# Performance work log

Hardware: AMD Instinct MI355X
Metric: run time of the kernel (lower is better)

The kernel has to match this reference:

```python
import jax, jax.numpy as jnp
from jax import lax
import numpy as np

M, CLS, K, DL, DC, DO, BD = 87, 65, 128, 128, 128, 2048, 256
B, H, W = 256, 7, 7


def _c1(x, Wt, b):
    # 1x1 Conv2d: [B,Cin,H,W] -> [B,Cout,H,W]
    return jnp.einsum('oc,bchw->bohw', Wt, x) + b[None, :, None, None]


def _pagerank(edge, v_init, p=0.85, iters=100):
    # torch: transition = adj / adj.sum(dim=1)  (broadcast divides COLUMNS by row-sums)
    n = edge.shape[0]
    Wpr = p * edge / jnp.sum(edge, axis=1)[None, :]
    s = v_init * n                                  # [B,n,1]
    coef = (1.0 - p) / n
    def body(i, xv):
        zx = coef * jnp.sum(xv, axis=1, keepdims=True)      # z_T @ x -> [B,1,1]
        return jnp.einsum('ij,bjo->bio', Wpr, xv) + s * zx
    xv = lax.fori_loop(0, iters, body, s)
    nrm = jnp.sqrt(jnp.sum(xv * xv, axis=1, keepdims=True))  # F.normalize(dim=1)
    xv = xv / jnp.maximum(nrm, 1e-12)
    return (v_init + xv).reshape(v_init.shape[0], -1)        # [B,n]


def setup_inputs() -> dict:
    key = jax.random.key(0)
    ks = jax.random.split(key, 24)
    def w(k, shape, s=0.02):
        return jax.random.normal(k, shape, jnp.float32) * s
    rng = np.random.default_rng(0)
    A = (rng.random((M, M)) < 0.08).astype(np.float32)
    A = np.maximum(A, A.T)
    np.fill_diagonal(A, 1.0)   # symmetric adjacency with self-loops (degrees > 0)
    return {
        'x': jax.random.normal(ks[0], (B, DO, H, W), jnp.float32),
        'Wb': w(ks[1], (BD, DO)), 'bb': w(ks[2], (BD,), 0.01),
        'Wfc': w(ks[3], (CLS, BD)), 'Wfc2': w(ks[4], (CLS, BD)),
        'Wo1': w(ks[5], (4 * DL, DO)), 'bo1': w(ks[6], (4 * DL,), 0.01),
        'Wo2': w(ks[7], (DL, 4 * DL)), 'bo2': w(ks[8], (DL,), 0.01),
        'Wa': w(ks[9], (M, DL)), 'ba': w(ks[10], (M,), 0.01),
        'Wps': w(ks[11], (DC, DL)), 'bps': w(ks[12], (DC,), 0.01),
        'node_p': jax.random.uniform(ks[13], (K, M), jnp.float32, -0.1, 0.1),
        'Wg': w(ks[14], (DC, DC + K)), 'bg': w(ks[15], (DC,), 0.01),
        'Wsp': w(ks[16], (DL, DC)), 'bsp': w(ks[17], (DL,), 0.01),
        'Ws': w(ks[18], (1, DC + DL)), 'bs': w(ks[19], (1,), 0.01),
        'Wox1': w(ks[20], (4 * DL, DL)), 'box1': w(ks[21], (4 * DL,), 0.01),
        'Wox2': w(ks[22], (DO, 4 * DL)), 'box2': w(ks[23], (DO,), 0.01),
        'edge': jnp.asarray(A),
    }


def reference(x, Wb, bb, Wfc, Wfc2, Wo1, bo1, Wo2, bo2, Wa, ba, Wps, bps,
              node_p, Wg, bg, Wsp, bsp, Ws, bs, Wox1, box1, Wox2, box2, edge):
    Bsz, _, hl, wl = x.shape
    HW = hl * wl

    # global pooled branch
    x_p = jnp.mean(x, axis=(2, 3))                           # [B,2048]
    features_p = x_p @ Wb.T + bb                             # [B,256]
    pre_output = features_p @ Wfc.T                          # [B,65]
    pre_score = jax.nn.softmax(lax.stop_gradient(pre_output), axis=1)

    # personalized pagerank over the semantic graph (constant wrt grads)
    v_init = jnp.concatenate(
        [jnp.zeros((Bsz, M - CLS), x.dtype), pre_score], axis=1)[:, :, None]
    v_y = lax.stop_gradient(_pagerank(edge, v_init))         # [B,87]

    # local feature reduction 2048 -> 512 -> 128
    x_l = _c1(_c1(x, Wo1, bo1), Wo2, bo2)                    # [B,128,7,7]

    a = _c1(x_l, Wa, ba).reshape(Bsz, M, HW).transpose(0, 2, 1)   # [B,HW,87]
    ps = _c1(x_l, Wps, bps).reshape(Bsz, DC, HW)                  # [B,128,HW]
    m1 = jax.nn.relu(jnp.matmul(ps, a))                           # [B,128,87]

    # replicate torch's exact (k, B*m) reshape + flat v_y broadcast
    node = jnp.broadcast_to(node_p[None], (Bsz, K, M)).reshape(K, Bsz * M)
    node = (v_y.reshape(-1) * node).reshape(Bsz, K, M)

    g = jnp.einsum('oc,bcm->bom', Wg, jnp.concatenate([node, m1], axis=1)) \
        + bg[None, :, None]                                   # [B,128,87]

    # D^-1/2 A D^-1/2 graph propagation
    Dinv = jnp.sum(edge, axis=0) ** -0.5
    edge_norm = Dinv[:, None] * edge * Dinv[None, :]
    m2 = jax.nn.relu(jnp.einsum('bcm,mn->bcn', g, edge_norm))  # [B,128,87]

    sp = jnp.einsum('oc,bcm->bom', Wsp, m2) + bsp[None, :, None]  # [B,128,87]

    # conv_s over concat(m2_expand, x_expand) is separable: avoid the
    # [B,256,HW,87] tensor entirely (1 output channel, 1x1 kernel).
    Ws1, Ws2 = Ws[0, :DC], Ws[0, DC:]
    t_node = jnp.einsum('c,bcm->bm', Ws1, m2)                  # [B,87]
    t_pix = jnp.einsum('c,bcp->bp', Ws2, x_l.reshape(Bsz, DL, HW))  # [B,HW]
    s_logits = t_node[:, :, None] + t_pix[:, None, :] + bs[0]  # [B,87,HW]
    s_att = jax.nn.softmax(s_logits, axis=1)                   # softmax over nodes

    m3 = jax.nn.relu(jnp.matmul(sp, s_att)).reshape(Bsz, DL, hl, wl)
    m3 = _c1(_c1(m3, Wox1, box1), Wox2, box2)                  # [B,2048,7,7]

    feature_aug = jnp.mean(m3, axis=(2, 3)) @ Wb.T + bb
    features = features_p + feature_aug
    outputs2 = features @ Wfc2.T
    softmax_outputs = jax.nn.softmax(outputs2, axis=1)
    return (features, outputs2, softmax_outputs, pre_output, features_p)
```

## Files before the change

### kernel.cpp

```cpp
#include <hip/hip_runtime.h>
#include <cmath>


typedef __attribute__((ext_vector_type(8))) short short8;
typedef __attribute__((ext_vector_type(4))) short s16x4;
typedef __attribute__((ext_vector_type(4))) float f32x4;

constexpr size_t OFF_W12BF = 0;
constexpr size_t OFF_T1BF  = 131072;
constexpr size_t OFF_WBBF  = 262144;
constexpr size_t OFF_XPBF  = 524288;
constexpr size_t OFF_WAPBF = 786432;
constexpr size_t OFF_WG2BF = 800768;
constexpr size_t OFF_ENPBF = 808960;
constexpr size_t OFF_B215  = 813568;
constexpr size_t OFF_B12   = 813792;
constexpr size_t OFF_WPR   = 813920;
constexpr size_t OFF_BTMP  = 821496;
constexpr size_t OFF_WC    = 823544;
constexpr size_t OFF_BC    = 856312;
constexpr size_t OFF_VY    = 856568;
constexpr size_t OFF_NT    = 878848;
constexpr size_t OFF_PART  = 901376;

__device__ __forceinline__ unsigned short f2bf(float f) {
  unsigned u = __builtin_bit_cast(unsigned, f);
  u += 0x7fffu + ((u >> 16) & 1u);
  return (unsigned short)(u >> 16);
}
__device__ __forceinline__ float bf2f(unsigned short s) {
  return __builtin_bit_cast(float, ((unsigned)s) << 16);
}

__global__ __launch_bounds__(256) void ksetup_all(
    const float* __restrict__ Wb,  const float* __restrict__ bb,
    const float* __restrict__ Wa,  const float* __restrict__ ba,
    const float* __restrict__ Wps, const float* __restrict__ bps,
    const float* __restrict__ Wg,  const float* __restrict__ edge,
    const float* __restrict__ Wo2, const float* __restrict__ Wo1,
    const float* __restrict__ Wox2,const float* __restrict__ Wox1,
    const float* __restrict__ box1,const float* __restrict__ box2,
    const float* __restrict__ bo1, const float* __restrict__ bo2,
    float* __restrict__ ws, float* __restrict__ featp)
{
  __shared__ alignas(16) short As[64*72];
  __shared__ alignas(16) short Bs[64*72];
  int blk = blockIdx.x, tid = threadIdx.x;
  if (blk < 2048) {
    int idx = blk*256 + tid;
    ((unsigned short*)(ws+OFF_WBBF))[idx] = f2bf(Wb[idx]);
  } else if (blk < 2304) {
    int idx = (blk-2048)*256 + tid;
    featp[idx] = bb[idx & 255];
  } else if (blk < 2432) {
    int idx = (blk-2304)*256 + tid;
    ws[OFF_WC + idx] = 0.f;
  } else if (blk < 2544) {
    int idx = (blk-2432)*256 + tid;
    int r = idx >> 7, c = idx & 127;
    float v;
    if (r < 128)      v = Wps[r*128 + c];
    else if (r < 215) v = Wa[(r-128)*128 + c];
    else              v = 0.f;
    ((unsigned short*)(ws+OFF_WAPBF))[idx] = f2bf(v);
  } else if (blk < 2608) {
    int idx = (blk-2544)*256 + tid;
    int o = idx >> 7, d = idx & 127;
    ((unsigned short*)(ws+OFF_WG2BF))[idx] = f2bf(Wg[o*256 + 128 + d]);
  } else if (blk < 2644) {
    int idx = (blk-2608)*256 + tid;
    int m = idx / 96, n = idx % 96;
    float v = 0.f;
    if (m < 87 && n < 87) {
      float sm = 0.f, sn = 0.f;
      for (int k = 0; k < 87; ++k) { sm += edge[k*87+m]; sn += edge[k*87+n]; }
      v = edge[m*87+n] / sqrtf(sm*sn);
    }
    ((unsigned short*)(ws+OFF_ENPBF))[idx] = f2bf(v);
  } else if (blk < 2674) {
    int idx = (blk-2644)*256 + tid;
    if (idx < 87*87) {
      int j = idx % 87;
      float rs = 0.f;
      for (int k = 0; k < 87; ++k) rs += edge[j*87+k];
      ws[OFF_WPR + idx] = 0.85f * edge[idx] / rs;
    }
  } else if (blk == 2674) {
    if (tid < 224) {
      float v = (tid < 128) ? bps[tid] : (tid < 215 ? ba[tid-128] : 0.f);
      ws[OFF_B215 + tid] = v;
    }
  } else if (blk < 2803) {
    int gb = blk - 2675;
    const float *A, *B; unsigned short* C; int lda, ldb, ldc, i0, j0;
    if (gb < 64) {
      A = Wo2; B = Wo1; C = (unsigned short*)(ws+OFF_W12BF);
      lda = 512; ldb = 2048; ldc = 2048;
      i0 = (gb & 1)*64; j0 = (gb >> 1)*64;
    } else {
      int b2 = gb - 64;
      A = Wox2; B = Wox1; C = (unsigned short*)(ws+OFF_T1BF);
      lda = 512; ldb = 128; ldc = 128;
      i0 = (b2 >> 1)*64; j0 = (b2 & 1)*64;
    }
    int w = tid >> 6, l = tid & 63, quad = l >> 4, lane16 = l & 15;
    f32x4 acc[4];
    #pragma unroll
    for (int i = 0; i < 4; ++i) acc[i] = (f32x4)(0.f);
    for (int kc = 0; kc < 512; kc += 64) {
      for (int t = tid; t < 1024; t += 256) {
        int r = t >> 4, k4 = t & 15;
        float4 v = *(const float4*)&A[(size_t)(i0+r)*lda + kc + k4*4];
        s16x4 sv; sv[0]=(short)f2bf(v.x); sv[1]=(short)f2bf(v.y); sv[2]=(short)f2bf(v.z); sv[3]=(short)f2bf(v.w);
        *(s16x4*)&As[r*72 + k4*4] = sv;
      }
      for (int t = tid; t < 1024; t += 256) {
        int kr = t >> 4, n4 = t & 15;
        float4 v = *(const float4*)&B[(size_t)(kc+kr)*ldb + j0 + n4*4];
        Bs[(n4*4+0)*72 + kr] = (short)f2bf(v.x);
        Bs[(n4*4+1)*72 + kr] = (short)f2bf(v.y);
        Bs[(n4*4+2)*72 + kr] = (short)f2bf(v.z);
        Bs[(n4*4+3)*72 + kr] = (short)f2bf(v.w);
      }
      __syncthreads();
      #pragma unroll
      for (int ks = 0; ks < 2; ++ks) {
        short8 a = *(const short8*)&As[(w*16+lane16)*72 + ks*32 + quad*8];
        #pragma unroll
        for (int nt = 0; nt < 4; ++nt) {
          short8 b8 = *(const short8*)&Bs[(nt*16+lane16)*72 + ks*32 + quad*8];
          acc[nt] = __builtin_amdgcn_mfma_f32_16x16x32_bf16(a, b8, acc[nt], 0, 0, 0);
        }
      }
      __syncthreads();
    }
    #pragma unroll
    for (int nt = 0; nt < 4; ++nt)
      #pragma unroll
      for (int r = 0; r < 4; ++r)
        C[(size_t)(i0 + w*16 + quad*4 + r)*ldc + j0 + nt*16 + lane16] = f2bf(acc[nt][r]);
  } else {
    int vb = blk - 2803;
    int w = tid >> 6, l = tid & 63;
    if (vb < 512) {
      int o = vb*4 + w;
      float s = 0.f;
      for (int h = l; h < 512; h += 64) s += Wox2[(size_t)o*512 + h] * box1[h];
      for (int off = 32; off; off >>= 1) s += __shfl_down(s, off, 64);
      if (l == 0) ws[OFF_BTMP + o] = s + box2[o];
    } else {
      int o = (vb - 512)*4 + w;
      float s = 0.f;
      for (int h = l; h < 512; h += 64) s += Wo2[(size_t)o*512 + h] * bo1[h];
      for (int off = 32; off; off >>= 1) s += __shfl_down(s, off, 64);
      if (l == 0) ws[OFF_B12 + o] = s + bo2[o];
    }
  }
}

__global__ __launch_bounds__(512, 6) void kmain5(const float* __restrict__ x,
                                                 const short* __restrict__ w12bf,
                                                 short* __restrict__ xpbf,
                                                 float* __restrict__ part)
{
  __shared__ alignas(16) short Bt[2][64*72];
  int b = blockIdx.x, q = blockIdx.y, tid = threadIdx.x;
  int w = tid >> 6, l = tid & 63;
  int quad = l >> 4, lane16 = l & 15;
  const float* xb = x + ((size_t)b*2048 + q*512)*49;

  int p4A = tid % 13, cA = tid / 13;
  int tB = tid + 512;
  int p4B = tB % 13, cB = tB / 13;
  bool hasB = (tid < 320);

  float fA[4], fB[4];
  {
    if (p4A < 12) {
      float4 v = *(const float4*)(xb + cA*49 + p4A*4);
      fA[0]=v.x; fA[1]=v.y; fA[2]=v.z; fA[3]=v.w;
    } else fA[0] = xb[cA*49 + 48];
    if (hasB) {
      if (p4B < 12) {
        float4 v = *(const float4*)(xb + cB*49 + p4B*4);
        fB[0]=v.x; fB[1]=v.y; fB[2]=v.z; fB[3]=v.w;
      } else fB[0] = xb[cB*49 + 48];
    }
  }

  f32x4 acc[4];
  #pragma unroll
  for (int i = 0; i < 4; ++i) acc[i] = (f32x4)(0.f);

  for (int kci = 0; kci < 8; ++kci) {
    short* bt = Bt[kci & 1];
    if (p4A < 12) {
      #pragma unroll
      for (int i = 0; i < 4; ++i) bt[(p4A*4+i)*72 + cA] = (short)f2bf(fA[i]);
    } else bt[48*72 + cA] = (short)f2bf(fA[0]);
    if (hasB) {
      if (p4B < 12) {
        #pragma unroll
        for (int i = 0; i < 4; ++i) bt[(p4B*4+i)*72 + cB] = (short)f2bf(fB[i]);
      } else bt[48*72 + cB] = (short)f2bf(fB[0]);
    }
    __syncthreads();
    if (kci < 7) {
      const float* xc = xb + (size_t)(kci+1)*64*49;
      if (p4A < 12) {
        float4 v = *(const float4*)(xc + cA*49 + p4A*4);
        fA[0]=v.x; fA[1]=v.y; fA[2]=v.z; fA[3]=v.w;
      } else fA[0] = xc[cA*49 + 48];
      if (hasB) {
        if (p4B < 12) {
          float4 v = *(const float4*)(xc + cB*49 + p4B*4);
          fB[0]=v.x; fB[1]=v.y; fB[2]=v.z; fB[3]=v.w;
        } else fB[0] = xc[cB*49 + 48];
      }
    }
    const short* wr = w12bf + (size_t)(w*16 + lane16)*2048 + q*512 + kci*64 + quad*8;
    short8 a0 = *(const short8*)(wr);
    short8 a1 = *(const short8*)(wr + 32);
    #pragma unroll
    for (int ni = 0; ni < 4; ++ni) {
      const short* br = bt + (ni*16 + lane16)*72 + quad*8;
      short8 b0 = *(const short8*)(br);
      short8 b1 = *(const short8*)(br + 32);
      acc[ni] = __builtin_amdgcn_mfma_f32_16x16x32_bf16(a0, b0, acc[ni], 0, 0, 0);
      acc[ni] = __builtin_amdgcn_mfma_f32_16x16x32_bf16(a1, b1, acc[ni], 0, 0, 0);
    }
    if (tid < 64) {
      float s = 0.f;
      for (int p = 0; p < 49; ++p)
        s += bf2f((unsigned short)bt[p*72 + tid]);
      xpbf[(size_t)b*2048 + q*512 + kci*64 + tid] = (short)f2bf(s * (1.f/49.f));
    }
  }
  float* po = part + ((size_t)q*256 + b)*6656;
  #pragma unroll
  for (int ni = 0; ni < 4; ++ni) {
    int p = ni*16 + lane16;
    if (p < 49) {
      #pragma unroll
      for (int r = 0; r < 4; ++r) {
        int o = w*16 + quad*4 + r;
        po[o*52 + p] = acc[ni][r];
      }
    }
  }
}

__global__ __launch_bounds__(256) void kwcf(const float* __restrict__ Wb,
                                            const float* __restrict__ bb,
                                            const short* __restrict__ xpbf,
                                            float* __restrict__ featp,
                                            float* __restrict__ ws)
{
  __shared__ alignas(16) short As[64*72];
  __shared__ alignas(16) short Bs[64*72];
  int blk = blockIdx.x, tid = threadIdx.x;
  if (blk < 64) {
    const short* wbbf = (const short*)(ws+OFF_WBBF);
    const short* t1s  = (const short*)(ws+OFF_T1BF);
    int i0 = (blk & 3)*64, j0 = ((blk >> 2) & 1)*64, kc0 = (blk >> 3)*256;
    int w = tid >> 6, l = tid & 63, quad = l >> 4, lane16 = l & 15;
    f32x4 acc[4];
    #pragma unroll
    for (int i = 0; i < 4; ++i) acc[i] = (f32x4)(0.f);
    for (int kc = kc0; kc < kc0+256; kc += 64) {
      for (int t = tid; t < 512; t += 256) {
        int r = t >> 3, c8 = t & 7;
        *(short8*)&As[r*72 + c8*8] = *(const short8*)&wbbf[(size_t)(i0+r)*2048 + kc + c8*8];
      }
      for (int t = tid; t < 1024; t += 256) {
        int kr = t >> 4, n4 = t & 15;
        s16x4 v = *(const s16x4*)&t1s[(size_t)(kc+kr)*128 + j0 + n4*4];
        Bs[(n4*4+0)*72 + kr] = v[0];
        Bs[(n4*4+1)*72 + kr] = v[1];
        Bs[(n4*4+2)*72 + kr] = v[2];
        Bs[(n4*4+3)*72 + kr] = v[3];
      }
      __syncthreads();
      #pragma unroll
      for (int ks = 0; ks < 2; ++ks) {
        short8 a = *(const short8*)&As[(w*16+lane16)*72 + ks*32 + quad*8];
        #pragma unroll
        for (int nt = 0; nt < 4; ++nt) {
          short8 b8 = *(const short8*)&Bs[(nt*16+lane16)*72 + ks*32 + quad*8];
          acc[nt] = __builtin_amdgcn_mfma_f32_16x16x32_bf16(a, b8, acc[nt], 0, 0, 0);
        }
      }
      __syncthreads();
    }
    #pragma unroll
    for (int nt = 0; nt < 4; ++nt)
      #pragma unroll
      for (int r = 0; r < 4; ++r)
        atomicAdd(&ws[OFF_WC + (size_t)(i0 + w*16 + quad*4 + r)*128 + j0 + nt*16 + lane16], acc[nt][r]);
  } else if (blk < 128) {
    int j = (blk-64)*4 + (tid >> 6), l = tid & 63;
    float s = 0.f;
    for (int c = l; c < 2048; c += 64) s += Wb[(size_t)j*2048 + c] * ws[OFF_BTMP + c];
    for (int off = 32; off; off >>= 1) s += __shfl_down(s, off, 64);
    if (l == 0) ws[OFF_BC + j] = s + bb[j];
  } else {
    const short* wbbf = (const short*)(ws+OFF_WBBF);
    int idx = blk - 128;
    int i0 = (idx & 3)*64, j0 = ((idx >> 2) & 3)*64, kc0 = (idx >> 4)*256;
    int w = tid >> 6, l = tid & 63, quad = l >> 4, lane16 = l & 15;
    f32x4 acc[4];
    #pragma unroll
    for (int i = 0; i < 4; ++i) acc[i] = (f32x4)(0.f);
    for (int kc = kc0; kc < kc0+256; kc += 32) {
      short8 a = *(const short8*)&xpbf[(size_t)(i0 + w*16 + lane16)*2048 + kc + quad*8];
      #pragma unroll
      for (int nt = 0; nt < 4; ++nt) {
        short8 b8 = *(const short8*)&wbbf[(size_t)(j0 + nt*16 + lane16)*2048 + kc + quad*8];
        acc[nt] = __builtin_amdgcn_mfma_f32_16x16x32_bf16(a, b8, acc[nt], 0, 0, 0);
      }
    }
    #pragma unroll
    for (int nt = 0; nt < 4; ++nt)
      #pragma unroll
      for (int r = 0; r < 4; ++r)
        atomicAdd(&featp[(size_t)(i0 + w*16 + quad*4 + r)*256 + j0 + nt*16 + lane16], acc[nt][r]);
  }
}

__global__ __launch_bounds__(384) void kpr(const float* __restrict__ featp,
                                           const float* __restrict__ Wfc,
                                           const float* __restrict__ wpr,
                                           float* __restrict__ preo,
                                           float* __restrict__ vy)
{
  __shared__ alignas(16) float fpr[256];
  __shared__ alignas(16) float po[68];
  __shared__ alignas(16) float vsA[88];
  __shared__ alignas(16) float vsB[88];
  __shared__ alignas(16) float vis[88];
  __shared__ float rd[4];
  int b = blockIdx.x, tid = threadIdx.x;
  if (tid < 256) fpr[tid] = featp[b*256 + tid];
  __syncthreads();
  if (tid < 260) {
    int row = tid >> 2, p = tid & 3;
    float s = 0.f;
    const float* wr = Wfc + row*256 + p*64;
    #pragma unroll
    for (int c = 0; c < 64; c += 4) {
      float4 w4 = *(const float4*)&wr[c];
      s += w4.x*fpr[p*64+c] + w4.y*fpr[p*64+c+1] + w4.z*fpr[p*64+c+2] + w4.w*fpr[p*64+c+3];
    }
    s += __shfl_xor(s, 1, 64);
    s += __shfl_xor(s, 2, 64);
    if (p == 0) { po[row] = s; preo[b*65 + row] = s; }
  }
  __syncthreads();
  if (tid < 64) {
    float v = po[tid];
    if (tid == 0) v = fmaxf(v, po[64]);
    float mx = v;
    #pragma unroll
    for (int off = 32; off; off >>= 1) mx = fmaxf(mx, __shfl_down(mx, off, 64));
    mx = __shfl(mx, 0, 64);
    float e = expf(po[tid]-mx) + ((tid == 0) ? expf(po[64]-mx) : 0.f);
    float sm = e;
    #pragma unroll
    for (int off = 32; off; off >>= 1) sm += __shfl_down(sm, off, 64);
    if (tid == 0) { rd[0] = mx; rd[1] = 1.f/sm; }
  }
  __syncthreads();
  if (tid < 88) {
    float vin = (tid >= 22 && tid < 87) ? expf(po[tid-22]-rd[0])*rd[1] : 0.f;
    vis[tid] = vin;
    vsA[tid] = vin * 87.f;
    vsB[tid] = 0.f;
  }
  __syncthreads();
  float wrow[22];
  const int m4 = tid >> 2, pp = tid & 3;
  if (tid < 348) {
    float add = vis[m4] * 0.15f;
    #pragma unroll
    for (int jj = 0; jj < 22; ++jj) {
      int j = pp*22 + jj;
      wrow[jj] = (j < 87) ? (wpr[m4*87 + j] + add) : 0.f;
    }
  }
  for (int it = 0; it < 64; ++it) {
    const float* vc = (it & 1) ? vsB : vsA;
    float* vn = (it & 1) ? vsA : vsB;
    if (tid < 348) {
      float nv = 0.f;
      #pragma unroll
      for (int jj = 0; jj < 22; ++jj) nv += wrow[jj] * vc[pp*22 + jj];
      nv += __shfl_xor(nv, 1, 64);
      nv += __shfl_xor(nv, 2, 64);
      if (pp == 0) vn[m4] = nv;
    }
    __syncthreads();
  }
  if (tid < 64) {
    float v = vsA[tid]*vsA[tid];
    if (tid < 23) v += vsA[64+tid]*vsA[64+tid];
    #pragma unroll
    for (int off = 32; off; off >>= 1) v += __shfl_down(v, off, 64);
    if (tid == 0) rd[2] = 1.f / fmaxf(sqrtf(v), 1e-12f);
  }
  __syncthreads();
  if (tid < 87) vy[b*87 + tid] = vis[tid] + vsA[tid]*rd[2];
}

__global__ __launch_bounds__(384) void knode(const float* __restrict__ Wg,
                                             const float* __restrict__ node_p,
                                             const float* __restrict__ vy,
                                             float* __restrict__ nt)
{
  int tid = threadIdx.x;
  if (tid >= 352) return;
  int out = blockIdx.x*88 + (tid >> 2);
  int par = out / 11264;
  int r = out % 11264;
  int o = r / 88, m = r % 88;
  int p = tid & 3;
  float s = 0.f;
  if (m < 87) {
    const float* vrow = vy + (size_t)(par*128)*87 + m;
    for (int k = p*32; k < p*32+32; ++k)
      s += Wg[o*256 + k] * node_p[k*87 + m] * vrow[k*87];
  }
  s += __shfl_xor(s, 1, 64);
  s += __shfl_xor(s, 2, 64);
  if (p == 0) nt[out] = s;
}

__global__ __launch_bounds__(512) void kgraph_all(
    const float* __restrict__ part,  const float* __restrict__ b12,
    const short* __restrict__ wapbf, const float* __restrict__ b215,
    const short* __restrict__ wg2bf, const float* __restrict__ nt,
    const float* __restrict__ bg,    const short* __restrict__ enpbf,
    const float* __restrict__ Wsp,   const float* __restrict__ bsp,
    const float* __restrict__ Ws,    const float* __restrict__ wc,
    const float* __restrict__ bc,    const float* __restrict__ featp,
    const float* __restrict__ Wfc2,
    float* __restrict__ feat, float* __restrict__ out2, float* __restrict__ soft)
{
  extern __shared__ char smraw[];
  short* XT = (short*)smraw;
  short* At = XT + 8704;
  short* M1 = At + 16128;
  short* G  = M1 + 13056;
  short* M2 = G  + 13312;
  float* fb  = (float*)(M2 + 13312);
  float* wsm = fb;
  float* tnb = fb + 96;
  float* zs  = fb + 192;
  float* m3s = fb + 320;
  float* fs  = fb + 448;
  float* o2s = fb + 704;
  float* red = fb + 776;

  int b = blockIdx.x, tid = threadIdx.x;
  int w = tid >> 6, l = tid & 63, quad = l >> 4, lane16 = l & 15;

  const float* p0 = part + (size_t)b*6656;
  const float* p1 = p0 + (size_t)256*6656;
  const float* p2 = p1 + (size_t)256*6656;
  const float* p3 = p2 + (size_t)256*6656;
  for (int t = tid; t < 6656; t += 512) {
    int o = t / 52, p = t % 52;
    XT[p*136 + o] = (short)f2bf(p0[t] + p1[t] + p2[t] + p3[t] + b12[o]);
  }
  for (int t = tid; t < 1536; t += 512) {
    int p = 52 + t/128, o = t % 128;
    XT[p*136 + o] = 0;
  }
  __syncthreads();

  for (int t = w; t < 56; t += 8) {
    int mt = t >> 2, n4 = t & 3;
    f32x4 acc = (f32x4)(0.f);
    #pragma unroll
    for (int ks = 0; ks < 4; ++ks) {
      short8 a  = *(const short8*)&wapbf[(size_t)(mt*16+lane16)*128 + ks*32 + quad*8];
      short8 b8 = *(const short8*)&XT[(n4*16+lane16)*136 + ks*32 + quad*8];
      acc = __builtin_amdgcn_mfma_f32_16x16x32_bf16(a, b8, acc, 0, 0, 0);
    }
    int p = n4*16 + lane16;
    #pragma unroll
    for (int r = 0; r < 4; ++r) {
      int rr = mt*16 + quad*4 + r;
      At[rr*72 + p] = (p < 49) ? (short)f2bf(acc[r] + b215[rr]) : (short)0;
    }
  }
  __syncthreads();

  for (int t = w; t < 48; t += 8) {
    int mt = t / 8, n4 = t % 8;
    f32x4 acc = (f32x4)(0.f);
    #pragma unroll
    for (int ks = 0; ks < 2; ++ks) {
      short8 a  = *(const short8*)&At[(128 + mt*16 + lane16)*72 + ks*32 + quad*8];
      short8 b8 = *(const short8*)&At[(n4*16+lane16)*72 + ks*32 + quad*8];
      acc = __builtin_amdgcn_mfma_f32_16x16x32_bf16(a, b8, acc, 0, 0, 0);
    }
    int d = n4*16 + lane16;
    #pragma unroll
    for (int r = 0; r < 4; ++r) {
      int m = mt*16 + quad*4 + r;
      M1[m*136 + d] = (short)f2bf(fmaxf(acc[r], 0.f));
    }
  }
  __syncthreads();

  const float* ntb = nt + (size_t)(b & 1)*11264;
  for (int t = w; t < 48; t += 8) {
    int mt = t / 6, n4 = t % 6;
    f32x4 acc = (f32x4)(0.f);
    #pragma unroll
    for (int ks = 0; ks < 4; ++ks) {
      short8 a  = *(const short8*)&wg2bf[(size_t)(mt*16+lane16)*128 + ks*32 + quad*8];
      short8 b8 = *(const short8*)&M1[(n4*16+lane16)*136 + ks*32 + quad*8];
      acc = __builtin_amdgcn_mfma_f32_16x16x32_bf16(a, b8, acc, 0, 0, 0);
    }
    int m = n4*16 + lane16;
    #pragma unroll
    for (int r = 0; r < 4; ++r) {
      int o = mt*16 + quad*4 + r;
      float v = acc[r] + bg[o] + ((m < 88) ? ntb[o*88 + m] : 0.f);
      G[o*104 + m] = (short)f2bf(v);
    }
  }
  __syncthreads();

  for (int t = w; t < 48; t += 8) {
    int mt = t / 6, n4 = t % 6;
    f32x4 acc = (f32x4)(0.f);
    #pragma unroll
    for (int ks = 0; ks < 3; ++ks) {
      short8 a  = *(const short8*)&G[(mt*16+lane16)*104 + ks*32 + quad*8];
      short8 b8 = *(const short8*)&enpbf[(size_t)(n4*16+lane16)*96 + ks*32 + quad*8];
      acc = __builtin_amdgcn_mfma_f32_16x16x32_bf16(a, b8, acc, 0, 0, 0);
    }
    int n = n4*16 + lane16;
    #pragma unroll
    for (int r = 0; r < 4; ++r) {
      int c = mt*16 + quad*4 + r;
      M2[c*104 + n] = (short)f2bf(fmaxf(acc[r], 0.f));
    }
  }
  __syncthreads();

  if (tid < 348) {
    int m = tid >> 2, p = tid & 3;
    float s = 0.f;
    for (int c = p*32; c < p*32+32; ++c)
      s += Ws[c] * bf2f((unsigned short)M2[c*104 + m]);
    s += __shfl_xor(s, 1, 64);
    s += __shfl_xor(s, 2, 64);
    if (p == 0) tnb[m] = s;
  }
  __syncthreads();
  if (tid < 64) {
    float v = tnb[tid];
    if (tid < 23) v = fmaxf(v, tnb[64+tid]);
    float mx = v;
    #pragma unroll
    for (int off = 32; off; off >>= 1) mx = fmaxf(mx, __shfl_down(mx, off, 64));
    mx = __shfl(mx, 0, 64);
    float e0 = expf(tnb[tid]-mx);
    float e1 = (tid < 23) ? expf(tnb[64+tid]-mx) : 0.f;
    float sm = e0 + e1;
    #pragma unroll
    for (int off = 32; off; off >>= 1) sm += __shfl_down(sm, off, 64);
    sm = __shfl(sm, 0, 64);
    float inv = 1.f/sm;
    wsm[tid] = e0*inv;
    if (tid < 23) wsm[64+tid] = e1*inv;
  }
  __syncthreads();
  {
    int c = tid >> 2, p = tid & 3;
    float s = 0.f;
    for (int mm = p*22; mm < p*22+22 && mm < 87; ++mm)
      s += bf2f((unsigned short)M2[c*104 + mm]) * wsm[mm];
    s += __shfl_xor(s, 1, 64);
    s += __shfl_xor(s, 2, 64);
    if (p == 0) zs[c] = s;
  }
  __syncthreads();
  {
    int d = tid >> 2, p = tid & 3;
    float s = 0.f;
    for (int c = p*32; c < p*32+32; ++c) s += Wsp[d*128 + c] * zs[c];
    s += __shfl_xor(s, 1, 64);
    s += __shfl_xor(s, 2, 64);
    if (p == 0) m3s[d] = fmaxf(s + bsp[d], 0.f);
  }
  __syncthreads();

  if (tid < 256) {
    float s = 0.f;
    #pragma unroll 4
    for (int d4 = 0; d4 < 32; ++d4) {
      float4 w4 = *(const float4*)&wc[tid*128 + d4*4];
      s += w4.x*m3s[d4*4] + w4.y*m3s[d4*4+1] + w4.z*m3s[d4*4+2] + w4.w*m3s[d4*4+3];
    }
    float f = featp[b*256 + tid] + bc[tid] + s;
    fs[tid] = f;
    feat[b*256 + tid] = f;
  }
  __syncthreads();
  if (tid < 260) {
    int row = tid >> 2, p = tid & 3;
    float s = 0.f;
    for (int c = p*64; c < p*64+64; c += 4) {
      float4 w4 = *(const float4*)&Wfc2[row*256 + c];
      s += w4.x*fs[c] + w4.y*fs[c+1] + w4.z*fs[c+2] + w4.w*fs[c+3];
    }
    s += __shfl_xor(s, 1, 64);
    s += __shfl_xor(s, 2, 64);
    if (p == 0) { out2[b*65 + row] = s; o2s[row] = s; }
  }
  __syncthreads();
  if (tid < 64) {
    float v = o2s[tid];
    if (tid == 0) v = fmaxf(v, o2s[64]);
    float mx = v;
    #pragma unroll
    for (int off = 32; off; off >>= 1) mx = fmaxf(mx, __shfl_down(mx, off, 64));
    mx = __shfl(mx, 0, 64);
    float e = expf(o2s[tid]-mx) + ((tid == 0) ? expf(o2s[64]-mx) : 0.f);
    float sm = e;
    #pragma unroll
    for (int off = 32; off; off >>= 1) sm += __shfl_down(sm, off, 64);
    if (tid == 0) { red[0] = mx; red[1] = 1.f/sm; }
  }
  __syncthreads();
  if (tid < 65) soft[b*65 + tid] = expf(o2s[tid]-red[0]) * red[1];
}

extern "C" void kernel_launch(void* const* d_in, const int* in_sizes, int n_in,
                              void* d_out, int out_size, void* d_ws, size_t ws_size,
                              hipStream_t stream)
{
  (void)in_sizes; (void)n_in; (void)out_size; (void)ws_size;
  const float* x      = (const float*)d_in[0];
  const float* Wb     = (const float*)d_in[1];
  const float* bb     = (const float*)d_in[2];
  const float* Wfc    = (const float*)d_in[3];
  const float* Wfc2   = (const float*)d_in[4];
  const float* Wo1    = (const float*)d_in[5];
  const float* bo1    = (const float*)d_in[6];
  const float* Wo2    = (const float*)d_in[7];
  const float* bo2    = (const float*)d_in[8];
  const float* Wa     = (const float*)d_in[9];
  const float* ba     = (const float*)d_in[10];
  const float* Wps    = (const float*)d_in[11];
  const float* bps    = (const float*)d_in[12];
  const float* node_p = (const float*)d_in[13];
  const float* Wg     = (const float*)d_in[14];
  const float* bg     = (const float*)d_in[15];
  const float* Wsp    = (const float*)d_in[16];
  const float* bsp    = (const float*)d_in[17];
  const float* Ws     = (const float*)d_in[18];
  const float* Wox1   = (const float*)d_in[20];
  const float* box1   = (const float*)d_in[21];
  const float* Wox2   = (const float*)d_in[22];
  const float* box2   = (const float*)d_in[23];
  const float* edge   = (const float*)d_in[24];

  float* ws   = (float*)d_ws;
  float* out  = (float*)d_out;
  float* feat  = out;
  float* out2  = out + 65536;
  float* soft  = out + 82176;
  float* preo  = out + 98816;
  float* featp = out + 115456;

  ksetup_all<<<3347, 256, 0, stream>>>(Wb, bb, Wa, ba, Wps, bps, Wg, edge,
                                       Wo2, Wo1, Wox2, Wox1, box1, box2, bo1, bo2,
                                       ws, featp);
  kmain5<<<dim3(256,4), 512, 0, stream>>>(x, (const short*)(ws + OFF_W12BF),
                                          (short*)(ws + OFF_XPBF), ws + OFF_PART);
  kwcf<<<256, 256, 0, stream>>>(Wb, bb, (const short*)(ws + OFF_XPBF), featp, ws);
  kpr<<<256, 384, 0, stream>>>(featp, Wfc, ws + OFF_WPR, preo, ws + OFF_VY);
  knode<<<256, 384, 0, stream>>>(Wg, node_p, ws + OFF_VY, ws + OFF_NT);
  kgraph_all<<<256, 512, 132144, stream>>>(ws + OFF_PART, ws + OFF_B12,
                                           (const short*)(ws + OFF_WAPBF),
                                           ws + OFF_B215,
                                           (const short*)(ws + OFF_WG2BF),
                                           ws + OFF_NT, bg,
                                           (const short*)(ws + OFF_ENPBF),
                                           Wsp, bsp, Ws,
                                           ws + OFF_WC, ws + OFF_BC, featp, Wfc2,
                                           feat, out2, soft);
}
```

Baseline: 331.1 us.

## Halve kmain5 K-split, precompute pooled partial sums, vectorize setup copies

The main GEMM kernel now splits the 2048-channel reduction into 2 chunks instead of 4, so each block loops over 16 K-tiles and the downstream graph kernel sums only two partial buffers. The per-channel spatial mean is computed from per-thread partial sums stored in a small shared buffer rather than by one thread serially reading 49 bf16 values, which also avoids bf16 rounding in the pool. The setup kernel's weight conversion, bias broadcast and zeroing paths use float4/short8 vector accesses with fewer blocks. The trade-off is fewer kmain5 blocks (512 vs 1024) with a lower occupancy hint and extra shared memory, against less partial-sum traffic.

```diff
diff --git a/kernel.cpp b/kernel.cpp
--- a/kernel.cpp
+++ b/kernel.cpp
@@ -46,29 +46,39 @@
   __shared__ alignas(16) short As[64*72];
   __shared__ alignas(16) short Bs[64*72];
   int blk = blockIdx.x, tid = threadIdx.x;
-  if (blk < 2048) {
-    int idx = blk*256 + tid;
-    ((unsigned short*)(ws+OFF_WBBF))[idx] = f2bf(Wb[idx]);
-  } else if (blk < 2304) {
-    int idx = (blk-2048)*256 + tid;
-    featp[idx] = bb[idx & 255];
-  } else if (blk < 2432) {
-    int idx = (blk-2304)*256 + tid;
-    ws[OFF_WC + idx] = 0.f;
-  } else if (blk < 2544) {
-    int idx = (blk-2432)*256 + tid;
-    int r = idx >> 7, c = idx & 127;
-    float v;
-    if (r < 128)      v = Wps[r*128 + c];
-    else if (r < 215) v = Wa[(r-128)*128 + c];
-    else              v = 0.f;
-    ((unsigned short*)(ws+OFF_WAPBF))[idx] = f2bf(v);
-  } else if (blk < 2608) {
-    int idx = (blk-2544)*256 + tid;
-    int o = idx >> 7, d = idx & 127;
-    ((unsigned short*)(ws+OFF_WG2BF))[idx] = f2bf(Wg[o*256 + 128 + d]);
-  } else if (blk < 2644) {
-    int idx = (blk-2608)*256 + tid;
+  if (blk < 256) {
+    int base = (blk*256 + tid)*8;
+    float4 v0 = *(const float4*)&Wb[base];
+    float4 v1 = *(const float4*)&Wb[base+4];
+    short8 sv;
+    sv[0]=(short)f2bf(v0.x); sv[1]=(short)f2bf(v0.y); sv[2]=(short)f2bf(v0.z); sv[3]=(short)f2bf(v0.w);
+    sv[4]=(short)f2bf(v1.x); sv[5]=(short)f2bf(v1.y); sv[6]=(short)f2bf(v1.z); sv[7]=(short)f2bf(v1.w);
+    *(short8*)&((unsigned short*)(ws+OFF_WBBF))[base] = sv;
+  } else if (blk < 320) {
+    int idx4 = ((blk-256)*256 + tid)*4;
+    float4 bv = *(const float4*)&bb[idx4 & 255];
+    *(float4*)&featp[idx4] = bv;
+  } else if (blk < 352) {
+    int idx4 = ((blk-320)*256 + tid)*4;
+    float4 z; z.x=z.y=z.z=z.w=0.f;
+    *(float4*)&ws[OFF_WC + idx4] = z;
+  } else if (blk < 380) {
+    int idx4 = ((blk-352)*256 + tid)*4;
+    int r = idx4 >> 7, c = idx4 & 127;
+    float4 v;
+    if (r < 128)      v = *(const float4*)&Wps[r*128 + c];
+    else if (r < 215) v = *(const float4*)&Wa[(r-128)*128 + c];
+    else              { v.x=v.y=v.z=v.w=0.f; }
+    s16x4 sv; sv[0]=(short)f2bf(v.x); sv[1]=(short)f2bf(v.y); sv[2]=(short)f2bf(v.z); sv[3]=(short)f2bf(v.w);
+    *(s16x4*)&((unsigned short*)(ws+OFF_WAPBF))[idx4] = sv;
+  } else if (blk < 396) {
+    int idx4 = ((blk-380)*256 + tid)*4;
+    int o = idx4 >> 7, d = idx4 & 127;
+    float4 v = *(const float4*)&Wg[o*256 + 128 + d];
+    s16x4 sv; sv[0]=(short)f2bf(v.x); sv[1]=(short)f2bf(v.y); sv[2]=(short)f2bf(v.z); sv[3]=(short)f2bf(v.w);
+    *(s16x4*)&((unsigned short*)(ws+OFF_WG2BF))[idx4] = sv;
+  } else if (blk < 432) {
+    int idx = (blk-396)*256 + tid;
     int m = idx / 96, n = idx % 96;
     float v = 0.f;
     if (m < 87 && n < 87) {
@@ -77,21 +87,21 @@
       v = edge[m*87+n] / sqrtf(sm*sn);
     }
     ((unsigned short*)(ws+OFF_ENPBF))[idx] = f2bf(v);
-  } else if (blk < 2674) {
-    int idx = (blk-2644)*256 + tid;
+  } else if (blk < 462) {
+    int idx = (blk-432)*256 + tid;
     if (idx < 87*87) {
       int j = idx % 87;
       float rs = 0.f;
       for (int k = 0; k < 87; ++k) rs += edge[j*87+k];
       ws[OFF_WPR + idx] = 0.85f * edge[idx] / rs;
     }
-  } else if (blk == 2674) {
+  } else if (blk == 462) {
     if (tid < 224) {
       float v = (tid < 128) ? bps[tid] : (tid < 215 ? ba[tid-128] : 0.f);
       ws[OFF_B215 + tid] = v;
     }
-  } else if (blk < 2803) {
-    int gb = blk - 2675;
+  } else if (blk < 591) {
+    int gb = blk - 463;
     const float *A, *B; unsigned short* C; int lda, ldb, ldc, i0, j0;
     if (gb < 64) {
       A = Wo2; B = Wo1; C = (unsigned short*)(ws+OFF_W12BF);
@@ -140,7 +150,7 @@
       for (int r = 0; r < 4; ++r)
         C[(size_t)(i0 + w*16 + quad*4 + r)*ldc + j0 + nt*16 + lane16] = f2bf(acc[nt][r]);
   } else {
-    int vb = blk - 2803;
+    int vb = blk - 591;
     int w = tid >> 6, l = tid & 63;
     if (vb < 512) {
       int o = vb*4 + w;
@@ -158,16 +168,17 @@
   }
 }
 
-__global__ __launch_bounds__(512, 6) void kmain5(const float* __restrict__ x,
+__global__ __launch_bounds__(512, 4) void kmain5(const float* __restrict__ x,
                                                  const short* __restrict__ w12bf,
                                                  short* __restrict__ xpbf,
                                                  float* __restrict__ part)
 {
   __shared__ alignas(16) short Bt[2][64*72];
+  __shared__ alignas(16) float xpp[2][832];
   int b = blockIdx.x, q = blockIdx.y, tid = threadIdx.x;
   int w = tid >> 6, l = tid & 63;
   int quad = l >> 4, lane16 = l & 15;
-  const float* xb = x + ((size_t)b*2048 + q*512)*49;
+  const float* xb = x + ((size_t)b*2048 + q*1024)*49;
 
   int p4A = tid % 13, cA = tid / 13;
   int tB = tid + 512;
@@ -192,20 +203,29 @@
   #pragma unroll
   for (int i = 0; i < 4; ++i) acc[i] = (f32x4)(0.f);
 
-  for (int kci = 0; kci < 8; ++kci) {
+  for (int kci = 0; kci < 16; ++kci) {
     short* bt = Bt[kci & 1];
+    float* xp = xpp[kci & 1];
     if (p4A < 12) {
       #pragma unroll
       for (int i = 0; i < 4; ++i) bt[(p4A*4+i)*72 + cA] = (short)f2bf(fA[i]);
-    } else bt[48*72 + cA] = (short)f2bf(fA[0]);
+      xp[tid] = fA[0]+fA[1]+fA[2]+fA[3];
+    } else {
+      bt[48*72 + cA] = (short)f2bf(fA[0]);
+      xp[tid] = fA[0];
+    }
     if (hasB) {
       if (p4B < 12) {
         #pragma unroll
         for (int i = 0; i < 4; ++i) bt[(p4B*4+i)*72 + cB] = (short)f2bf(fB[i]);
-      } else bt[48*72 + cB] = (short)f2bf(fB[0]);
+        xp[512 + tid] = fB[0]+fB[1]+fB[2]+fB[3];
+      } else {
+        bt[48*72 + cB] = (short)f2bf(fB[0]);
+        xp[512 + tid] = fB[0];
+      }
     }
     __syncthreads();
-    if (kci < 7) {
+    if (kci < 15) {
       const float* xc = xb + (size_t)(kci+1)*64*49;
       if (p4A < 12) {
         float4 v = *(const float4*)(xc + cA*49 + p4A*4);
@@ -218,7 +238,7 @@
         } else fB[0] = xc[cB*49 + 48];
       }
     }
-    const short* wr = w12bf + (size_t)(w*16 + lane16)*2048 + q*512 + kci*64 + quad*8;
+    const short* wr = w12bf + (size_t)(w*16 + lane16)*2048 + q*1024 + kci*64 + quad*8;
     short8 a0 = *(const short8*)(wr);
     short8 a1 = *(const short8*)(wr + 32);
     #pragma unroll
@@ -231,9 +251,9 @@
     }
     if (tid < 64) {
       float s = 0.f;
-      for (int p = 0; p < 49; ++p)
-        s += bf2f((unsigned short)bt[p*72 + tid]);
-      xpbf[(size_t)b*2048 + q*512 + kci*64 + tid] = (short)f2bf(s * (1.f/49.f));
+      #pragma unroll
+      for (int j = 0; j < 13; ++j) s += xp[tid*13 + j];
+      xpbf[(size_t)b*2048 + q*1024 + kci*64 + tid] = (short)f2bf(s * (1.f/49.f));
     }
   }
   float* po = part + ((size_t)q*256 + b)*6656;
@@ -465,11 +485,9 @@
 
   const float* p0 = part + (size_t)b*6656;
   const float* p1 = p0 + (size_t)256*6656;
-  const float* p2 = p1 + (size_t)256*6656;
-  const float* p3 = p2 + (size_t)256*6656;
   for (int t = tid; t < 6656; t += 512) {
     int o = t / 52, p = t % 52;
-    XT[p*136 + o] = (short)f2bf(p0[t] + p1[t] + p2[t] + p3[t] + b12[o]);
+    XT[p*136 + o] = (short)f2bf(p0[t] + p1[t] + b12[o]);
   }
   for (int t = tid; t < 1536; t += 512) {
     int p = 52 + t/128, o = t % 128;
@@ -678,10 +696,10 @@
   float* preo  = out + 98816;
   float* featp = out + 115456;
 
-  ksetup_all<<<3347, 256, 0, stream>>>(Wb, bb, Wa, ba, Wps, bps, Wg, edge,
+  ksetup_all<<<1135, 256, 0, stream>>>(Wb, bb, Wa, ba, Wps, bps, Wg, edge,
                                        Wo2, Wo1, Wox2, Wox1, box1, box2, bo1, bo2,
                                        ws, featp);
-  kmain5<<<dim3(256,4), 512, 0, stream>>>(x, (const short*)(ws + OFF_W12BF),
+  kmain5<<<dim3(256,2), 512, 0, stream>>>(x, (const short*)(ws + OFF_W12BF),
                                           (short*)(ws + OFF_XPBF), ws + OFF_PART);
   kwcf<<<256, 256, 0, stream>>>(Wb, bb, (const short*)(ws + OFF_XPBF), featp, ws);
   kpr<<<256, 384, 0, stream>>>(featp, Wfc, ws + OFF_WPR, preo, ws + OFF_VY);
```

New measurement: 336.7 us. About the same (+1.7%).
